# Optimization experiments

Hardware: AMD Instinct MI355X
Metric: run time of the kernel (lower is better)

The kernel has to match this reference:

```python
import jax, jax.numpy as jnp
import numpy as np

WS = 8       # window_size
SHIFT = 4    # shift_size = window_size // 2
NH = 12      # num_heads


def setup_inputs() -> dict:
    key = jax.random.key(0)
    k0, k1, k2 = jax.random.split(key, 3)
    B, N, E = 32, 3136, 384
    x = jax.random.normal(k0, (B, N, E), dtype=jnp.float32)
    w_qkv = jax.random.normal(k1, (3 * E, E), dtype=jnp.float32) * 0.02
    b_qkv = jnp.zeros((3 * E,), dtype=jnp.float32)
    w_out = jax.random.normal(k2, (E, E), dtype=jnp.float32) * 0.02
    b_out = jnp.zeros((E,), dtype=jnp.float32)
    return {"x": x, "w_qkv": w_qkv, "b_qkv": b_qkv, "w_out": w_out, "b_out": b_out}


def reference(x, w_qkv, b_qkv, w_out, b_out):
    B, N, E = x.shape
    H = W = int(np.sqrt(N))
    hd = E // NH
    scale = np.float32(1.0 / np.sqrt(hd))

    xg = x.reshape(B, H, W, E)
    # cyclic shift
    xg = jnp.roll(xg, shift=(-SHIFT, -SHIFT), axis=(1, 2))
    nh_w, nw_w = H // WS, W // WS
    # window partition -> [B*num_windows, ws*ws, E]
    xw = (xg.reshape(B, nh_w, WS, nw_w, WS, E)
            .transpose(0, 1, 3, 2, 4, 5)
            .reshape(B * nh_w * nw_w, WS * WS, E))

    # fused qkv projection (torch in_proj layout: [3E, E])
    qkv = xw @ w_qkv.T + b_qkv          # [Bw, T, 3E]
    q, k, v = jnp.split(qkv, 3, axis=-1)

    def to_heads(t):
        return t.reshape(t.shape[0], WS * WS, NH, hd).transpose(0, 2, 1, 3)  # [Bw, H, T, hd]

    q, k, v = to_heads(q), to_heads(k), to_heads(v)
    scores = jnp.einsum('bhqd,bhkd->bhqk', q, k) * scale
    attn = jax.nn.softmax(scores, axis=-1)
    o = jnp.einsum('bhqk,bhkd->bhqd', attn, v)            # [Bw, H, T, hd]
    o = o.transpose(0, 2, 1, 3).reshape(-1, WS * WS, E)   # merge heads
    o = o @ w_out.T + b_out

    # window reverse + reverse cyclic shift
    o = (o.reshape(B, nh_w, nw_w, WS, WS, E)
           .transpose(0, 1, 3, 2, 4, 5)
           .reshape(B, H, W, E))
    o = jnp.roll(o, shift=(SHIFT, SHIFT), axis=(1, 2))
    return o.reshape(B, N, E)
```

## Files before the change

kernel.cpp:

```cpp
#include <hip/hip_runtime.h>

typedef short short8 __attribute__((ext_vector_type(8)));
typedef float floatx4 __attribute__((ext_vector_type(4)));

#define DI __device__ __forceinline__

constexpr int Bn   = 32;
constexpr int HW   = 56;
constexpr int E    = 384;
constexpr int E3   = 1152;
constexpr int NHd  = 12;
constexpr int HD   = 32;
constexpr int SH   = 4;
constexpr int T    = 64;
constexpr int NWIN = Bn * 7 * 7;
constexpr int MROW = NWIN * T;
constexpr int OS   = E3;

DI unsigned short f2bf(float f) {
  unsigned int u = __builtin_bit_cast(unsigned int, f);
  u = u + 0x7FFFu + ((u >> 16) & 1u);
  return (unsigned short)(u >> 16);
}

#define GLOAD_LDS16(gsrc, ldst)                                                     \
  __builtin_amdgcn_global_load_lds(                                                 \
      (const __attribute__((address_space(1))) unsigned int*)(gsrc),                \
      (__attribute__((address_space(3))) unsigned int*)(ldst), 16, 0, 0)

__global__ void cast_all(const float* __restrict__ x,
                         const float* __restrict__ wqkv,
                         const float* __restrict__ wout,
                         unsigned short* __restrict__ x_bf,
                         unsigned short* __restrict__ wqkv_bf,
                         unsigned short* __restrict__ wout_bf) {
  const size_t QX = (size_t)Bn * 3136 * E / 4;
  const size_t Q1 = QX + (size_t)E3 * E / 4;
  const size_t Q2 = Q1 + (size_t)E * E / 4;
  for (size_t i = (size_t)blockIdx.x * 256 + threadIdx.x; i < Q2;
       i += (size_t)gridDim.x * 256) {
    const float* s; unsigned short* d; size_t j;
    if (i < QX)      { s = x;    d = x_bf;    j = i; }
    else if (i < Q1) { s = wqkv; d = wqkv_bf; j = i - QX; }
    else             { s = wout; d = wout_bf; j = i - Q1; }
    const float4 v = *reinterpret_cast<const float4*>(s + j * 4);
    ushort4 h;
    h.x = f2bf(v.x); h.y = f2bf(v.y); h.z = f2bf(v.z); h.w = f2bf(v.w);
    *reinterpret_cast<ushort4*>(d + j * 4) = h;
  }
}

__global__ __launch_bounds__(256, 2)
void qkv_gemm(const unsigned short* __restrict__ x_bf,
              const unsigned short* __restrict__ wqkv,
              const float* __restrict__ bqkv,
              unsigned short* __restrict__ qkv) {
  __shared__ unsigned short As[128 * 64];
  __shared__ unsigned short Bs[128 * 64];

  const int tid  = threadIdx.x;
  const int wave = tid >> 6, lane = tid & 63;
  const int quad = lane >> 4, l16 = lane & 15;
  const int wm = wave >> 1, wn = wave & 1;

  const int orig = blockIdx.x;
  const int wgid = (orig & 7) * 882 + (orig >> 3);
  const int m0 = (wgid / 9) * 128, n0 = (wgid % 9) * 128;

  const unsigned short* asrc[4];
  const unsigned short* bsrc[4];
  #pragma unroll
  for (int it = 0; it < 4; ++it) {
    int f = tid + it * 256;
    int row = f >> 3;
    int clog = (f & 7) ^ (row & 7);
    int m = m0 + row;
    int win = m >> 6, t = m & 63;
    int b = win / 49, wrem = win % 49;
    int wi = wrem / 7, wj = wrem % 7;
    int ti = t >> 3, tj = t & 7;
    int gi = (wi * 8 + ti + SH) % HW;
    int gj = (wj * 8 + tj + SH) % HW;
    asrc[it] = x_bf + (size_t)(b * 3136 + gi * 56 + gj) * E + clog * 8;
    bsrc[it] = wqkv + (size_t)(n0 + row) * E + clog * 8;
  }

  const floatx4 zero4 = {0.f, 0.f, 0.f, 0.f};
  floatx4 acc[4][4];
  #pragma unroll
  for (int mt = 0; mt < 4; ++mt)
    #pragma unroll
    for (int nt = 0; nt < 4; ++nt) acc[mt][nt] = zero4;

  for (int kb = 0; kb < 6; ++kb) {
    #pragma unroll
    for (int it = 0; it < 4; ++it) {
      GLOAD_LDS16(asrc[it] + kb * 64, As + it * 2048 + wave * 512);
      GLOAD_LDS16(bsrc[it] + kb * 64, Bs + it * 2048 + wave * 512);
    }
    __syncthreads();
    #pragma unroll
    for (int kk = 0; kk < 2; ++kk) {
      short8 af[4], bf[4];
      #pragma unroll
      for (int mt = 0; mt < 4; ++mt)
        af[mt] = *reinterpret_cast<const short8*>(
            &As[(wm * 64 + mt * 16 + l16) * 64 + (((kk * 4 + quad) ^ (l16 & 7)) * 8)]);
      #pragma unroll
      for (int nt = 0; nt < 4; ++nt)
        bf[nt] = *reinterpret_cast<const short8*>(
            &Bs[(wn * 64 + nt * 16 + l16) * 64 + (((kk * 4 + quad) ^ (l16 & 7)) * 8)]);
      #pragma unroll
      for (int mt = 0; mt < 4; ++mt)
        #pragma unroll
        for (int nt = 0; nt < 4; ++nt)
          acc[mt][nt] = __builtin_amdgcn_mfma_f32_16x16x32_bf16(af[mt], bf[nt], acc[mt][nt], 0, 0, 0);
    }
    __syncthreads();
  }

  #pragma unroll
  for (int nt = 0; nt < 4; ++nt) {
    int col = n0 + wn * 64 + nt * 16 + l16;
    float bias = bqkv[col];
    #pragma unroll
    for (int mt = 0; mt < 4; ++mt) {
      #pragma unroll
      for (int r = 0; r < 4; ++r) {
        int m = m0 + wm * 64 + mt * 16 + quad * 4 + r;
        qkv[(size_t)m * OS + col] = f2bf(acc[mt][nt][r] + bias);
      }
    }
  }
}

__global__ __launch_bounds__(64)
void attn(unsigned short* __restrict__ qkv) {
  __shared__ unsigned short smem[7424];
  unsigned short* qs = smem;
  unsigned short* ks = smem + 2560;
  unsigned short* ps = smem;
  unsigned short* vT = smem + 5120;

  const int lane = threadIdx.x;
  const int quad = lane >> 4, l16 = lane & 15;
  const int wh  = blockIdx.x;
  const int win = wh / NHd, h = wh % NHd;
  const size_t base = (size_t)win * T * OS;
  const int hoff = h * HD;

  #pragma unroll
  for (int it = 0; it < 4; ++it) {
    int c = it * 64 + lane;
    int row = c >> 2, cc = c & 3;
    size_t roff = base + (size_t)row * OS + hoff + cc * 8;
    *reinterpret_cast<short8*>(&qs[row * 40 + cc * 8]) =
        *reinterpret_cast<const short8*>(qkv + roff);
    *reinterpret_cast<short8*>(&ks[row * 40 + cc * 8]) =
        *reinterpret_cast<const short8*>(qkv + roff + E);
  }
  #pragma unroll
  for (int it = 0; it < 4; ++it) {
    int c = it * 64 + lane;
    int t = c >> 2, dc = c & 3;
    short8 vv = *reinterpret_cast<const short8*>(
        qkv + base + (size_t)t * OS + 2 * E + hoff + dc * 8);
    #pragma unroll
    for (int j = 0; j < 8; ++j) vT[(dc * 8 + j) * 72 + t] = (unsigned short)vv[j];
  }
  __syncthreads();

  const floatx4 zero4 = {0.f, 0.f, 0.f, 0.f};

  short8 aq[4];
  #pragma unroll
  for (int mt = 0; mt < 4; ++mt)
    aq[mt] = *reinterpret_cast<const short8*>(&qs[(mt * 16 + l16) * 40 + quad * 8]);
  floatx4 sacc[4][4];
  #pragma unroll
  for (int nt = 0; nt < 4; ++nt) {
    short8 bk = *reinterpret_cast<const short8*>(&ks[(nt * 16 + l16) * 40 + quad * 8]);
    #pragma unroll
    for (int mt = 0; mt < 4; ++mt)
      sacc[mt][nt] = __builtin_amdgcn_mfma_f32_16x16x32_bf16(aq[mt], bk, zero4, 0, 0, 0);
  }
  __syncthreads();

  const float scale = 0.17677669529663687f;
  #pragma unroll
  for (int mt = 0; mt < 4; ++mt) {
    #pragma unroll
    for (int r = 0; r < 4; ++r) {
      float s0 = sacc[mt][0][r] * scale, s1 = sacc[mt][1][r] * scale;
      float s2 = sacc[mt][2][r] * scale, s3 = sacc[mt][3][r] * scale;
      float mx = fmaxf(fmaxf(s0, s1), fmaxf(s2, s3));
      #pragma unroll
      for (int off = 1; off < 16; off <<= 1) mx = fmaxf(mx, __shfl_xor(mx, off, 64));
      float e0 = __expf(s0 - mx), e1 = __expf(s1 - mx);
      float e2 = __expf(s2 - mx), e3 = __expf(s3 - mx);
      float sm = e0 + e1 + e2 + e3;
      #pragma unroll
      for (int off = 1; off < 16; off <<= 1) sm += __shfl_xor(sm, off, 64);
      float inv = 1.0f / sm;
      int row = mt * 16 + quad * 4 + r;
      ps[row * 72 +  0 + l16] = f2bf(e0 * inv);
      ps[row * 72 + 16 + l16] = f2bf(e1 * inv);
      ps[row * 72 + 32 + l16] = f2bf(e2 * inv);
      ps[row * 72 + 48 + l16] = f2bf(e3 * inv);
    }
  }
  __syncthreads();

  #pragma unroll
  for (int mt = 0; mt < 4; ++mt) {
    floatx4 o0 = zero4, o1 = zero4;
    #pragma unroll
    for (int kk = 0; kk < 2; ++kk) {
      short8 ap = *reinterpret_cast<const short8*>(&ps[(mt * 16 + l16) * 72 + kk * 32 + quad * 8]);
      short8 b0 = *reinterpret_cast<const short8*>(&vT[(l16) * 72 + kk * 32 + quad * 8]);
      short8 b1 = *reinterpret_cast<const short8*>(&vT[(16 + l16) * 72 + kk * 32 + quad * 8]);
      o0 = __builtin_amdgcn_mfma_f32_16x16x32_bf16(ap, b0, o0, 0, 0, 0);
      o1 = __builtin_amdgcn_mfma_f32_16x16x32_bf16(ap, b1, o1, 0, 0, 0);
    }
    #pragma unroll
    for (int r = 0; r < 4; ++r) {
      int tok = mt * 16 + quad * 4 + r;
      qkv[base + (size_t)tok * OS + hoff + l16]      = f2bf(o0[r]);
      qkv[base + (size_t)tok * OS + hoff + 16 + l16] = f2bf(o1[r]);
    }
  }
}

__global__ __launch_bounds__(256, 2)
void out_proj(const unsigned short* __restrict__ o_ws,
              const unsigned short* __restrict__ wout,
              const float* __restrict__ bout,
              float* __restrict__ out) {
  __shared__ unsigned short As[128 * 64];
  __shared__ unsigned short Bs[128 * 64];

  const int tid  = threadIdx.x;
  const int wave = tid >> 6, lane = tid & 63;
  const int quad = lane >> 4, l16 = lane & 15;
  const int wm = wave >> 1, wn = wave & 1;

  const int orig = blockIdx.x;
  const int wgid = (orig & 7) * 294 + (orig >> 3);
  const int m0 = (wgid / 3) * 128, n0 = (wgid % 3) * 128;

  const unsigned short* asrc[4];
  const unsigned short* bsrc[4];
  #pragma unroll
  for (int it = 0; it < 4; ++it) {
    int f = tid + it * 256;
    int row = f >> 3;
    int clog = (f & 7) ^ (row & 7);
    asrc[it] = o_ws + (size_t)(m0 + row) * OS + clog * 8;
    bsrc[it] = wout + (size_t)(n0 + row) * E + clog * 8;
  }

  const floatx4 zero4 = {0.f, 0.f, 0.f, 0.f};
  floatx4 acc[4][4];
  #pragma unroll
  for (int mt = 0; mt < 4; ++mt)
    #pragma unroll
    for (int nt = 0; nt < 4; ++nt) acc[mt][nt] = zero4;

  for (int kb = 0; kb < 6; ++kb) {
    #pragma unroll
    for (int it = 0; it < 4; ++it) {
      GLOAD_LDS16(asrc[it] + kb * 64, As + it * 2048 + wave * 512);
      GLOAD_LDS16(bsrc[it] + kb * 64, Bs + it * 2048 + wave * 512);
    }
    __syncthreads();
    #pragma unroll
    for (int kk = 0; kk < 2; ++kk) {
      short8 af[4], bf[4];
      #pragma unroll
      for (int mt = 0; mt < 4; ++mt)
        af[mt] = *reinterpret_cast<const short8*>(
            &As[(wm * 64 + mt * 16 + l16) * 64 + (((kk * 4 + quad) ^ (l16 & 7)) * 8)]);
      #pragma unroll
      for (int nt = 0; nt < 4; ++nt)
        bf[nt] = *reinterpret_cast<const short8*>(
            &Bs[(wn * 64 + nt * 16 + l16) * 64 + (((kk * 4 + quad) ^ (l16 & 7)) * 8)]);
      #pragma unroll
      for (int mt = 0; mt < 4; ++mt)
        #pragma unroll
        for (int nt = 0; nt < 4; ++nt)
          acc[mt][nt] = __builtin_amdgcn_mfma_f32_16x16x32_bf16(af[mt], bf[nt], acc[mt][nt], 0, 0, 0);
    }
    __syncthreads();
  }

  #pragma unroll
  for (int nt = 0; nt < 4; ++nt) {
    int col = n0 + wn * 64 + nt * 16 + l16;
    float bias = bout[col];
    #pragma unroll
    for (int mt = 0; mt < 4; ++mt) {
      #pragma unroll
      for (int r = 0; r < 4; ++r) {
        int m = m0 + wm * 64 + mt * 16 + quad * 4 + r;
        int win = m >> 6, t = m & 63;
        int bb = win / 49, wrem = win % 49;
        int wi = wrem / 7, wj = wrem % 7;
        int ti = t >> 3, tj = t & 7;
        int gi = (wi * 8 + ti + SH) % HW;
        int gj = (wj * 8 + tj + SH) % HW;
        out[(size_t)(bb * 3136 + gi * 56 + gj) * E + col] = acc[mt][nt][r] + bias;
      }
    }
  }
}

extern "C" void kernel_launch(void* const* d_in, const int* in_sizes, int n_in,
                              void* d_out, int out_size, void* d_ws, size_t ws_size,
                              hipStream_t stream) {
  (void)in_sizes; (void)n_in; (void)out_size;
  const float* x    = (const float*)d_in[0];
  const float* wqkv = (const float*)d_in[1];
  const float* bqkv = (const float*)d_in[2];
  const float* wout = (const float*)d_in[3];
  const float* bout = (const float*)d_in[4];
  float* out = (float*)d_out;

  unsigned short* wqkv_bf = (unsigned short*)d_ws;
  unsigned short* wout_bf = wqkv_bf + (size_t)E3 * E;
  unsigned short* qkv_ws  = wout_bf + (size_t)E * E;

  const size_t xbf_elems = (size_t)Bn * 3136 * E;
  const size_t need_elems = (size_t)E3 * E + (size_t)E * E +
                            (size_t)MROW * E3 + xbf_elems;
  unsigned short* x_bf;
  if (ws_size >= need_elems * sizeof(unsigned short))
    x_bf = qkv_ws + (size_t)MROW * E3;
  else
    x_bf = (unsigned short*)d_out;

  cast_all<<<2048, 256, 0, stream>>>(x, wqkv, wout, x_bf, wqkv_bf, wout_bf);
  qkv_gemm<<<7056, 256, 0, stream>>>(x_bf, wqkv_bf, bqkv, qkv_ws);
  attn<<<NWIN * NHd, 64, 0, stream>>>(qkv_ws);
  out_proj<<<2352, 256, 0, stream>>>(qkv_ws, wout_bf, bout, out);
}
```

Before: 541.4 us.

## Store QKV in per-window-head contiguous layout so attention loads directly to registers

The QKV GEMM epilogue now scatters its outputs into a [window, head, q/k/v, token, dim] layout, so each attention block reads contiguous 4 KB slabs. With that layout, Q and K fragments are loaded straight from global memory into MFMA registers, which removes the LDS staging and two barriers. The attention output is written back into the Q slot, and out_proj's A-operand addressing follows the new layout by stepping over head pairs. In exchange, the GEMM epilogue stores become more scattered, and out_proj's A loads now jump between head slabs.

After: 520.0 us. 4.0% less time.

```diff
diff --git a/kernel.cpp b/kernel.cpp
--- a/kernel.cpp
+++ b/kernel.cpp
@@ -15,7 +15,8 @@
 constexpr int T    = 64;
 constexpr int NWIN = Bn * 7 * 7;
 constexpr int MROW = NWIN * T;
-constexpr int OS   = E3;
+
+constexpr int SB   = 2048;
 
 DI unsigned short f2bf(float f) {
   unsigned int u = __builtin_bit_cast(unsigned int, f);
@@ -123,12 +124,17 @@
   for (int nt = 0; nt < 4; ++nt) {
     int col = n0 + wn * 64 + nt * 16 + l16;
     float bias = bqkv[col];
+    int qi = col / 384;
+    int hcol = col - qi * 384;
+    int hh = hcol >> 5, d = hcol & 31;
     #pragma unroll
     for (int mt = 0; mt < 4; ++mt) {
       #pragma unroll
       for (int r = 0; r < 4; ++r) {
         int m = m0 + wm * 64 + mt * 16 + quad * 4 + r;
-        qkv[(size_t)m * OS + col] = f2bf(acc[mt][nt][r] + bias);
+        int win = m >> 6, t = m & 63;
+        qkv[((size_t)(win * NHd + hh) * 3 + qi) * SB + t * 32 + d] =
+            f2bf(acc[mt][nt][r] + bias);
       }
     }
   }
@@ -136,55 +142,43 @@
 
 __global__ __launch_bounds__(64)
 void attn(unsigned short* __restrict__ qkv) {
-  __shared__ unsigned short smem[7424];
-  unsigned short* qs = smem;
-  unsigned short* ks = smem + 2560;
+  __shared__ unsigned short smem[6912];
   unsigned short* ps = smem;
-  unsigned short* vT = smem + 5120;
+  unsigned short* vT = smem + 4608;
 
   const int lane = threadIdx.x;
   const int quad = lane >> 4, l16 = lane & 15;
   const int wh  = blockIdx.x;
   const int win = wh / NHd, h = wh % NHd;
-  const size_t base = (size_t)win * T * OS;
-  const int hoff = h * HD;
-
-  #pragma unroll
-  for (int it = 0; it < 4; ++it) {
-    int c = it * 64 + lane;
-    int row = c >> 2, cc = c & 3;
-    size_t roff = base + (size_t)row * OS + hoff + cc * 8;
-    *reinterpret_cast<short8*>(&qs[row * 40 + cc * 8]) =
-        *reinterpret_cast<const short8*>(qkv + roff);
-    *reinterpret_cast<short8*>(&ks[row * 40 + cc * 8]) =
-        *reinterpret_cast<const short8*>(qkv + roff + E);
-  }
+  const size_t bq = (size_t)(win * NHd + h) * 3 * SB;
+
   #pragma unroll
   for (int it = 0; it < 4; ++it) {
     int c = it * 64 + lane;
     int t = c >> 2, dc = c & 3;
-    short8 vv = *reinterpret_cast<const short8*>(
-        qkv + base + (size_t)t * OS + 2 * E + hoff + dc * 8);
+    short8 vv = *reinterpret_cast<const short8*>(qkv + bq + 2 * SB + c * 8);
     #pragma unroll
     for (int j = 0; j < 8; ++j) vT[(dc * 8 + j) * 72 + t] = (unsigned short)vv[j];
   }
-  __syncthreads();
+
+  short8 aq[4], bk[4];
+  #pragma unroll
+  for (int mt = 0; mt < 4; ++mt)
+    aq[mt] = *reinterpret_cast<const short8*>(
+        qkv + bq + (size_t)(mt * 16 + l16) * 32 + quad * 8);
+  #pragma unroll
+  for (int nt = 0; nt < 4; ++nt)
+    bk[nt] = *reinterpret_cast<const short8*>(
+        qkv + bq + SB + (size_t)(nt * 16 + l16) * 32 + quad * 8);
 
   const floatx4 zero4 = {0.f, 0.f, 0.f, 0.f};
 
-  short8 aq[4];
-  #pragma unroll
-  for (int mt = 0; mt < 4; ++mt)
-    aq[mt] = *reinterpret_cast<const short8*>(&qs[(mt * 16 + l16) * 40 + quad * 8]);
   floatx4 sacc[4][4];
   #pragma unroll
-  for (int nt = 0; nt < 4; ++nt) {
-    short8 bk = *reinterpret_cast<const short8*>(&ks[(nt * 16 + l16) * 40 + quad * 8]);
+  for (int nt = 0; nt < 4; ++nt)
     #pragma unroll
     for (int mt = 0; mt < 4; ++mt)
-      sacc[mt][nt] = __builtin_amdgcn_mfma_f32_16x16x32_bf16(aq[mt], bk, zero4, 0, 0, 0);
-  }
-  __syncthreads();
+      sacc[mt][nt] = __builtin_amdgcn_mfma_f32_16x16x32_bf16(aq[mt], bk[nt], zero4, 0, 0, 0);
 
   const float scale = 0.17677669529663687f;
   #pragma unroll
@@ -225,8 +219,8 @@
     #pragma unroll
     for (int r = 0; r < 4; ++r) {
       int tok = mt * 16 + quad * 4 + r;
-      qkv[base + (size_t)tok * OS + hoff + l16]      = f2bf(o0[r]);
-      qkv[base + (size_t)tok * OS + hoff + 16 + l16] = f2bf(o1[r]);
+      qkv[bq + tok * 32 + l16]      = f2bf(o0[r]);
+      qkv[bq + tok * 32 + 16 + l16] = f2bf(o1[r]);
     }
   }
 }
@@ -255,7 +249,10 @@
     int f = tid + it * 256;
     int row = f >> 3;
     int clog = (f & 7) ^ (row & 7);
-    asrc[it] = o_ws + (size_t)(m0 + row) * OS + clog * 8;
+    int m = m0 + row;
+    int win = m >> 6, t = m & 63;
+    int h0 = clog >> 2, d0 = (clog & 3) * 8;
+    asrc[it] = o_ws + (size_t)(win * NHd + h0) * 3 * SB + t * 32 + d0;
     bsrc[it] = wout + (size_t)(n0 + row) * E + clog * 8;
   }
 
@@ -269,7 +266,7 @@
   for (int kb = 0; kb < 6; ++kb) {
     #pragma unroll
     for (int it = 0; it < 4; ++it) {
-      GLOAD_LDS16(asrc[it] + kb * 64, As + it * 2048 + wave * 512);
+      GLOAD_LDS16(asrc[it] + kb * (2 * 3 * SB), As + it * 2048 + wave * 512);
       GLOAD_LDS16(bsrc[it] + kb * 64, Bs + it * 2048 + wave * 512);
     }
     __syncthreads();
```
